# Optimization experiments

Hardware: AMD Instinct MI355X
Metric: run time of the kernel (lower is better)

## Reference

```python
import jax, jax.numpy as jnp
import numpy as np

N_NODES = 100000
N_EDGES = 3200000
F_IN = 128
F_OUT = 128


def setup_inputs() -> dict:
    key = jax.random.key(0)
    ks = jax.random.split(key, 6)
    stdv = 1.0 / np.sqrt(F_OUT)
    return {
        "x": jax.random.normal(ks[0], (N_NODES, F_IN), dtype=jnp.float32),
        "weight": jax.random.uniform(ks[1], (F_IN, F_OUT), minval=-stdv, maxval=stdv, dtype=jnp.float32),
        "bias": jax.random.uniform(ks[2], (F_OUT,), minval=-stdv, maxval=stdv, dtype=jnp.float32),
        "edge_src": jax.random.randint(ks[3], (N_EDGES,), 0, N_NODES, dtype=jnp.int32),
        "edge_dst": jax.random.randint(ks[4], (N_EDGES,), 0, N_NODES, dtype=jnp.int32),
        "edge_weight": jax.random.uniform(ks[5], (N_EDGES,), dtype=jnp.float32),
    }


def reference(x, weight, bias, edge_src, edge_dst, edge_weight):
    # Dense feature transform: support = X @ W  -> [N, F_OUT]
    support = jnp.matmul(x, weight)
    # Sparse adjacency aggregation (SpMM): out[d] = sum_e A[d, s_e] * support[s_e]
    msgs = support[edge_src] * edge_weight[:, None]  # [E, F_OUT]
    out = jax.ops.segment_sum(msgs, edge_dst, num_segments=N_NODES)
    return out + bias
```

## Files before the change

kernel.cpp:

```cpp
#include <hip/hip_runtime.h>

#define F 128
#define NB 64
#define MAXB 2048
#define NCHUNK 256

typedef __bf16 bf16x8 __attribute__((ext_vector_type(8)));
typedef unsigned short u16x8 __attribute__((ext_vector_type(8)));
typedef float f32x4 __attribute__((ext_vector_type(4)));

static __device__ __forceinline__ unsigned short f2bf(float f) {
    unsigned u = __float_as_uint(f);
    unsigned r = (u + 0x7FFF + ((u >> 16) & 1)) >> 16;
    return (unsigned short)r;
}

__global__ __launch_bounds__(256) void gemm_mfma_kernel(const float* __restrict__ X,
                                                        const float* __restrict__ W,
                                                        unsigned short* __restrict__ Sb,
                                                        int n_nodes) {
    __shared__ unsigned short WT[F * F];
    int t = threadIdx.x;
    {
        int f = t >> 1, half = t & 1;
#pragma unroll
        for (int j = 0; j < 8; ++j) {
            int k0 = half * 64 + j * 8;
            u16x8 pk;
#pragma unroll
            for (int i = 0; i < 8; ++i) pk[i] = f2bf(W[(size_t)(k0 + i) * F + f]);
            int byte = f * 256 + ((k0 * 2) ^ ((f & 7) << 4));
            *(u16x8*)((char*)WT + byte) = pk;
        }
    }
    __syncthreads();

    int w = t >> 6, l = t & 63;
    int lr = l & 15, lg = l >> 4;
    int rowBase = blockIdx.x * 64 + w * 16;

    f32x4 acc[8] = {};
    int a_row = rowBase + lr;
    if (a_row >= n_nodes) a_row = n_nodes - 1;
    const float* arow = X + (size_t)a_row * F + lg * 8;

#pragma unroll
    for (int kt = 0; kt < 4; ++kt) {
        const float* ap = arow + kt * 32;
        float4 x0 = *(const float4*)ap;
        float4 x1 = *(const float4*)(ap + 4);
        u16x8 au;
        au[0] = f2bf(x0.x); au[1] = f2bf(x0.y); au[2] = f2bf(x0.z); au[3] = f2bf(x0.w);
        au[4] = f2bf(x1.x); au[5] = f2bf(x1.y); au[6] = f2bf(x1.z); au[7] = f2bf(x1.w);
        bf16x8 a = __builtin_bit_cast(bf16x8, au);
#pragma unroll
        for (int ct = 0; ct < 8; ++ct) {
            int f = ct * 16 + lr;
            int byte = f * 256 + (((kt * 32 + lg * 8) * 2) ^ ((f & 7) << 4));
            bf16x8 b = *(bf16x8*)((char*)WT + byte);
            acc[ct] = __builtin_amdgcn_mfma_f32_16x16x32_bf16(a, b, acc[ct], 0, 0, 0);
        }
    }

#pragma unroll
    for (int ct = 0; ct < 8; ++ct) {
        int col = ct * 16 + lr;
#pragma unroll
        for (int j = 0; j < 4; ++j) {
            int row = rowBase + lg * 4 + j;
            if (row < n_nodes) Sb[(size_t)row * F + col] = f2bf(acc[ct][j]);
        }
    }
}

__global__ __launch_bounds__(256) void chunk_hist_kernel(const int* __restrict__ edst,
                                                         int* __restrict__ counts,
                                                         int* __restrict__ bcnt,
                                                         int n_edges, int nbuck, int epc) {
    __shared__ int h[MAXB];
    int c = blockIdx.x, t = threadIdx.x;
    for (int i = t; i < nbuck; i += 256) h[i] = 0;
    __syncthreads();
    int beg = c * epc, end = min(n_edges, beg + epc);
    for (int e = beg + t; e < end; e += 256) {
        atomicAdd(&h[edst[e] >> 6], 1);
    }
    __syncthreads();
    for (int i = t; i < nbuck; i += 256) {
        int v = h[i];
        counts[(size_t)c * nbuck + i] = v;
        if (v) __hip_atomic_fetch_add(&bcnt[i], v, __ATOMIC_RELAXED, __HIP_MEMORY_SCOPE_AGENT);
    }
}

__global__ __launch_bounds__(256) void bscan_kernel(const int* __restrict__ bcnt,
                                                    int* __restrict__ bstart, int nbuck) {
    __shared__ int tsum[256];
    int t = threadIdx.x;
    const int EPT = MAXB / 256;
    int base = t * EPT;
    int v[EPT];
    int s = 0;
#pragma unroll
    for (int i = 0; i < EPT; ++i) {
        int idx = base + i;
        v[i] = (idx < nbuck) ? bcnt[idx] : 0;
        s += v[i];
    }
    tsum[t] = s;
    __syncthreads();
    for (int off = 1; off < 256; off <<= 1) {
        int x = (t >= off) ? tsum[t - off] : 0;
        __syncthreads();
        tsum[t] += x;
        __syncthreads();
    }
    int run = tsum[t] - s;
#pragma unroll
    for (int i = 0; i < EPT; ++i) {
        int idx = base + i;
        if (idx < nbuck) {
            bstart[idx] = run;
            run += v[i];
        }
    }
    if (t == 255) bstart[nbuck] = run;
}

__global__ __launch_bounds__(64) void chunk_offs_kernel(const int* __restrict__ counts,
                                                        const int* __restrict__ bstart,
                                                        int* __restrict__ offs, int nbuck) {
    int b = blockIdx.x * 64 + threadIdx.x;
    if (b >= nbuck) return;
    int run = bstart[b];
    for (int c = 0; c < NCHUNK; ++c) {
        int v = counts[(size_t)c * nbuck + b];
        offs[(size_t)c * nbuck + b] = run;
        run += v;
    }
}

__global__ __launch_bounds__(256) void chunk_scatter_kernel(const int* __restrict__ esrc,
                                                            const int* __restrict__ edst,
                                                            const float* __restrict__ ew,
                                                            const int* __restrict__ offs,
                                                            int2* __restrict__ ebuf,
                                                            int n_edges, int nbuck, int epc) {
    __shared__ int lcur[MAXB];
    int c = blockIdx.x, t = threadIdx.x;
    for (int i = t; i < nbuck; i += 256) lcur[i] = offs[(size_t)c * nbuck + i];
    __syncthreads();
    int beg = c * epc, end = min(n_edges, beg + epc);
    for (int e = beg + t; e < end; e += 256) {
        int d = edst[e];
        int pos = atomicAdd(&lcur[d >> 6], 1);
        int2 p;
        p.x = esrc[e] | ((d & (NB - 1)) << 20);
        p.y = __float_as_int(ew[e]);
        ebuf[pos] = p;
    }
}

__global__ __launch_bounds__(256) void local_sort_kernel(const int2* __restrict__ ebuf,
                                                         const int* __restrict__ bstart,
                                                         int2* __restrict__ csr,
                                                         int* __restrict__ rowst,
                                                         int* __restrict__ cnt_out, int n_nodes) {
    __shared__ int lcnt[NB];
    __shared__ int lcur[NB];
    int b = blockIdx.x, t = threadIdx.x;
    int beg = bstart[b], end = bstart[b + 1];

    if (t < NB) lcnt[t] = 0;
    __syncthreads();

    for (int e = beg + t; e < end; e += 256) {
        int dl = (ebuf[e].x >> 20) & (NB - 1);
        atomicAdd(&lcnt[dl], 1);
    }
    __syncthreads();

    if (t < NB) {
        int v = lcnt[t];
        int inc = v;
#pragma unroll
        for (int off = 1; off < NB; off <<= 1) {
            int up = __shfl_up(inc, off, NB);
            if (t >= off) inc += up;
        }
        int excl = inc - v;
        lcur[t] = excl;
        int node = b * NB + t;
        if (node < n_nodes) {
            rowst[node] = beg + excl;
            cnt_out[node] = v;
        }
    }
    __syncthreads();

    for (int e = beg + t; e < end; e += 256) {
        int2 p = ebuf[e];
        int dl = (p.x >> 20) & (NB - 1);
        int pos = beg + atomicAdd(&lcur[dl], 1);
        int2 q;
        q.x = p.x & 0xFFFFF;
        q.y = p.y;
        csr[pos] = q;
    }
}

__global__ __launch_bounds__(256) void gather_kernel(const unsigned short* __restrict__ Sb,
                                                     const int2* __restrict__ csr,
                                                     const int* __restrict__ rowst,
                                                     const int* __restrict__ cnt,
                                                     const float* __restrict__ bias,
                                                     float* __restrict__ out, int n_nodes) {
    int node = blockIdx.x * 4 + (threadIdx.x >> 6);
    if (node >= n_nodes) return;
    int lane = threadIdx.x & 63;
    int f0 = lane * 2;

    float2 acc = *(const float2*)&bias[f0];
    int beg = rowst[node];
    int num = cnt[node];

    int i = 0;
    for (; i + 8 <= num; i += 8) {
        unsigned g[8];
        float wv[8];
#pragma unroll
        for (int j = 0; j < 8; ++j) {
            int2 p = csr[beg + i + j];
            g[j] = *(const unsigned*)(Sb + (size_t)p.x * F + f0);
            wv[j] = __int_as_float(p.y);
        }
#pragma unroll
        for (int j = 0; j < 8; ++j) {
            acc.x += wv[j] * __uint_as_float(g[j] << 16);
            acc.y += wv[j] * __uint_as_float(g[j] & 0xFFFF0000u);
        }
    }
    for (; i < num; ++i) {
        int2 p = csr[beg + i];
        unsigned g = *(const unsigned*)(Sb + (size_t)p.x * F + f0);
        float w = __int_as_float(p.y);
        acc.x += w * __uint_as_float(g << 16);
        acc.y += w * __uint_as_float(g & 0xFFFF0000u);
    }
    *(float2*)&out[(size_t)node * F + f0] = acc;
}

__global__ __launch_bounds__(256) void init_out_kernel(float* __restrict__ out,
                                                       const float* __restrict__ bias,
                                                       int n_nodes) {
    int idx = blockIdx.x * blockDim.x + threadIdx.x;
    int total = n_nodes * F;
    if (idx < total) out[idx] = bias[idx & (F - 1)];
}

__global__ __launch_bounds__(256) void scatter_edges_kernel(const unsigned short* __restrict__ Sb,
                                                            const int* __restrict__ esrc,
                                                            const int* __restrict__ edst,
                                                            const float* __restrict__ ew,
                                                            float* __restrict__ out,
                                                            int n_edges) {
    long long idx = (long long)blockIdx.x * blockDim.x + threadIdx.x;
    int e = (int)(idx >> 5);
    if (e >= n_edges) return;
    int fbase = ((int)idx & 31) * 4;
    int s = esrc[e];
    int d = edst[e];
    float w = ew[e];
    ushort4 v = *(const ushort4*)&Sb[(size_t)s * F + fbase];
    float* o = out + (size_t)d * F + fbase;
    __hip_atomic_fetch_add(&o[0], w * __uint_as_float((unsigned)v.x << 16), __ATOMIC_RELAXED, __HIP_MEMORY_SCOPE_AGENT);
    __hip_atomic_fetch_add(&o[1], w * __uint_as_float((unsigned)v.y << 16), __ATOMIC_RELAXED, __HIP_MEMORY_SCOPE_AGENT);
    __hip_atomic_fetch_add(&o[2], w * __uint_as_float((unsigned)v.z << 16), __ATOMIC_RELAXED, __HIP_MEMORY_SCOPE_AGENT);
    __hip_atomic_fetch_add(&o[3], w * __uint_as_float((unsigned)v.w << 16), __ATOMIC_RELAXED, __HIP_MEMORY_SCOPE_AGENT);
}

extern "C" void kernel_launch(void* const* d_in, const int* in_sizes, int n_in,
                              void* d_out, int out_size, void* d_ws, size_t ws_size,
                              hipStream_t stream) {
    const float* x    = (const float*)d_in[0];
    const float* w    = (const float*)d_in[1];
    const float* bias = (const float*)d_in[2];
    const int*   esrc = (const int*)d_in[3];
    const int*   edst = (const int*)d_in[4];
    const float* ew   = (const float*)d_in[5];
    float* out = (float*)d_out;

    int n_nodes = in_sizes[0] / F;
    int n_edges = in_sizes[3];
    int nbuck = (n_nodes + NB - 1) / NB;
    int epc = (n_edges + NCHUNK - 1) / NCHUNK;

    size_t off = 0;
    auto carve = [&](size_t bytes) -> void* {
        void* p = (char*)d_ws + off;
        off += (bytes + 255) & ~(size_t)255;
        return p;
    };
    unsigned short* Sb    = (unsigned short*)carve((size_t)n_nodes * F * sizeof(unsigned short));
    int2*           ebuf  = (int2*)carve((size_t)n_edges * sizeof(int2));
    int2*           csr   = (int2*)carve((size_t)n_edges * sizeof(int2));
    int*            bcnt  = (int*)carve((size_t)nbuck * sizeof(int));
    int*            bst   = (int*)carve((size_t)(nbuck + 1) * sizeof(int));
    int*            rowst = (int*)carve((size_t)n_nodes * sizeof(int));
    int*            ncnt  = (int*)carve((size_t)n_nodes * sizeof(int));
    int*            counts = (int*)carve((size_t)NCHUNK * nbuck * sizeof(int));
    int*            offs   = (int*)carve((size_t)NCHUNK * nbuck * sizeof(int));
    bool ok = (off <= ws_size) && (nbuck <= MAXB) && (n_nodes < (1 << 20));

    gemm_mfma_kernel<<<(n_nodes + 63) / 64, 256, 0, stream>>>(x, w, Sb, n_nodes);

    if (ok) {
        hipMemsetAsync(bcnt, 0, (size_t)nbuck * sizeof(int), stream);
        chunk_hist_kernel<<<NCHUNK, 256, 0, stream>>>(edst, counts, bcnt, n_edges, nbuck, epc);
        bscan_kernel<<<1, 256, 0, stream>>>(bcnt, bst, nbuck);
        chunk_offs_kernel<<<(nbuck + 63) / 64, 64, 0, stream>>>(counts, bst, offs, nbuck);
        chunk_scatter_kernel<<<NCHUNK, 256, 0, stream>>>(esrc, edst, ew, offs, ebuf,
                                                         n_edges, nbuck, epc);
        local_sort_kernel<<<nbuck, 256, 0, stream>>>(ebuf, bst, csr, rowst, ncnt, n_nodes);
        gather_kernel<<<(n_nodes + 3) / 4, 256, 0, stream>>>(Sb, csr, rowst, ncnt, bias, out,
                                                             n_nodes);
    } else {
        int total = n_nodes * F;
        init_out_kernel<<<(total + 255) / 256, 256, 0, stream>>>(out, bias, n_nodes);
        long long t2 = (long long)n_edges * 32;
        scatter_edges_kernel<<<(int)((t2 + 255) / 256), 256, 0, stream>>>(Sb, esrc, edst, ew, out,
                                                                          n_edges);
    }
}
```

Before: 252.1 us.

## Sort edges by source tile within rows, parallelize chunk offsets, nontemporal CSR loads

The local sort now keys each edge by destination node and by a coarse source-node tile (16 tiles). Within each row, gathered source rows are therefore ordered by source region, which should improve L2 locality across concurrent gather waves. The per-bucket chunk-offset scan now runs with 4 thread groups, each handling a quarter of the chunks with a shared-memory partial-sum combine, where before a single serial loop of 256 chunks ran per bucket. The gather reads CSR entries with nontemporal loads so they do not evict the support matrix from cache. The cost is a 1024-key block scan per bucket in local_sort.

```diff
diff --git a/kernel.cpp b/kernel.cpp
--- a/kernel.cpp
+++ b/kernel.cpp
@@ -4,6 +4,8 @@
 #define NB 64
 #define MAXB 2048
 #define NCHUNK 256
+#define NT 16
+#define KEYS (NB * NT)
 
 typedef __bf16 bf16x8 __attribute__((ext_vector_type(8)));
 typedef unsigned short u16x8 __attribute__((ext_vector_type(8)));
@@ -127,16 +129,27 @@
     if (t == 255) bstart[nbuck] = run;
 }
 
-__global__ __launch_bounds__(64) void chunk_offs_kernel(const int* __restrict__ counts,
-                                                        const int* __restrict__ bstart,
-                                                        int* __restrict__ offs, int nbuck) {
-    int b = blockIdx.x * 64 + threadIdx.x;
-    if (b >= nbuck) return;
-    int run = bstart[b];
-    for (int c = 0; c < NCHUNK; ++c) {
-        int v = counts[(size_t)c * nbuck + b];
-        offs[(size_t)c * nbuck + b] = run;
-        run += v;
+__global__ __launch_bounds__(256) void chunk_offs_kernel(const int* __restrict__ counts,
+                                                         const int* __restrict__ bstart,
+                                                         int* __restrict__ offs, int nbuck) {
+    __shared__ int part[4][64];
+    int t = threadIdx.x;
+    int q = t >> 6, bb = t & 63;
+    int b = blockIdx.x * 64 + bb;
+    int s = 0;
+    if (b < nbuck) {
+        for (int c = q * 64; c < q * 64 + 64; ++c) s += counts[(size_t)c * nbuck + b];
+    }
+    part[q][bb] = s;
+    __syncthreads();
+    if (b < nbuck) {
+        int run = bstart[b];
+        for (int qq = 0; qq < q; ++qq) run += part[qq][bb];
+        for (int c = q * 64; c < q * 64 + 64; ++c) {
+            size_t idx = (size_t)c * nbuck + b;
+            offs[idx] = run;
+            run += counts[idx];
+        }
     }
 }
 
@@ -165,45 +178,65 @@
                                                          const int* __restrict__ bstart,
                                                          int2* __restrict__ csr,
                                                          int* __restrict__ rowst,
-                                                         int* __restrict__ cnt_out, int n_nodes) {
-    __shared__ int lcnt[NB];
-    __shared__ int lcur[NB];
+                                                         int* __restrict__ cnt_out,
+                                                         int n_nodes, int ts) {
+    __shared__ int lcnt[KEYS];
+    __shared__ int lcur[KEYS];
+    __shared__ int tsum[256];
     int b = blockIdx.x, t = threadIdx.x;
     int beg = bstart[b], end = bstart[b + 1];
 
-    if (t < NB) lcnt[t] = 0;
+#pragma unroll
+    for (int i = t; i < KEYS; i += 256) lcnt[i] = 0;
     __syncthreads();
 
     for (int e = beg + t; e < end; e += 256) {
-        int dl = (ebuf[e].x >> 20) & (NB - 1);
-        atomicAdd(&lcnt[dl], 1);
+        int px = ebuf[e].x;
+        int key = ((px >> 20) & (NB - 1)) * NT + ((px & 0xFFFFF) >> ts);
+        atomicAdd(&lcnt[key], 1);
+    }
+    __syncthreads();
+
+    const int EPT = KEYS / 256;
+    int base = t * EPT;
+    int v[EPT];
+    int s = 0;
+#pragma unroll
+    for (int i = 0; i < EPT; ++i) { v[i] = lcnt[base + i]; s += v[i]; }
+    tsum[t] = s;
+    __syncthreads();
+    for (int off = 1; off < 256; off <<= 1) {
+        int x = (t >= off) ? tsum[t - off] : 0;
+        __syncthreads();
+        tsum[t] += x;
+        __syncthreads();
+    }
+    int run = tsum[t] - s;
+#pragma unroll
+    for (int i = 0; i < EPT; ++i) {
+        lcnt[base + i] = run;
+        lcur[base + i] = beg + run;
+        run += v[i];
     }
     __syncthreads();
 
     if (t < NB) {
-        int v = lcnt[t];
-        int inc = v;
-#pragma unroll
-        for (int off = 1; off < NB; off <<= 1) {
-            int up = __shfl_up(inc, off, NB);
-            if (t >= off) inc += up;
-        }
-        int excl = inc - v;
-        lcur[t] = excl;
         int node = b * NB + t;
         if (node < n_nodes) {
-            rowst[node] = beg + excl;
-            cnt_out[node] = v;
-        }
-    }
-    __syncthreads();
+            int p0 = lcnt[t * NT];
+            int p1 = (t == NB - 1) ? (end - beg) : lcnt[(t + 1) * NT];
+            rowst[node] = beg + p0;
+            cnt_out[node] = p1 - p0;
+        }
+    }
 
     for (int e = beg + t; e < end; e += 256) {
         int2 p = ebuf[e];
-        int dl = (p.x >> 20) & (NB - 1);
-        int pos = beg + atomicAdd(&lcur[dl], 1);
+        int src = p.x & 0xFFFFF;
+        int key = ((p.x >> 20) & (NB - 1)) * NT + (src >> ts);
+        int pos = atomicAdd(&lcur[key], 1);
         int2 q;
-        q.x = p.x & 0xFFFFF;
+        q.x = src;
         q.y = p.y;
         csr[pos] = q;
     }
@@ -230,9 +263,10 @@
         float wv[8];
 #pragma unroll
         for (int j = 0; j < 8; ++j) {
-            int2 p = csr[beg + i + j];
-            g[j] = *(const unsigned*)(Sb + (size_t)p.x * F + f0);
-            wv[j] = __int_as_float(p.y);
+            long long raw = __builtin_nontemporal_load((const long long*)&csr[beg + i + j]);
+            int srcj = (int)(raw & 0xFFFFFFFFll);
+            g[j] = *(const unsigned*)(Sb + (size_t)srcj * F + f0);
+            wv[j] = __int_as_float((int)(raw >> 32));
         }
 #pragma unroll
         for (int j = 0; j < 8; ++j) {
@@ -241,9 +275,10 @@
         }
     }
     for (; i < num; ++i) {
-        int2 p = csr[beg + i];
-        unsigned g = *(const unsigned*)(Sb + (size_t)p.x * F + f0);
-        float w = __int_as_float(p.y);
+        long long raw = __builtin_nontemporal_load((const long long*)&csr[beg + i]);
+        int srcj = (int)(raw & 0xFFFFFFFFll);
+        unsigned g = *(const unsigned*)(Sb + (size_t)srcj * F + f0);
+        float w = __int_as_float((int)(raw >> 32));
         acc.x += w * __uint_as_float(g << 16);
         acc.y += w * __uint_as_float(g & 0xFFFF0000u);
     }
@@ -295,6 +330,9 @@
     int nbuck = (n_nodes + NB - 1) / NB;
     int epc = (n_edges + NCHUNK - 1) / NCHUNK;
 
+    int ts = 0;
+    while (((n_nodes - 1) >> ts) >= NT) ++ts;
+
     size_t off = 0;
     auto carve = [&](size_t bytes) -> void* {
         void* p = (char*)d_ws + off;
@@ -318,10 +356,10 @@
         hipMemsetAsync(bcnt, 0, (size_t)nbuck * sizeof(int), stream);
         chunk_hist_kernel<<<NCHUNK, 256, 0, stream>>>(edst, counts, bcnt, n_edges, nbuck, epc);
         bscan_kernel<<<1, 256, 0, stream>>>(bcnt, bst, nbuck);
-        chunk_offs_kernel<<<(nbuck + 63) / 64, 64, 0, stream>>>(counts, bst, offs, nbuck);
+        chunk_offs_kernel<<<(nbuck + 63) / 64, 256, 0, stream>>>(counts, bst, offs, nbuck);
         chunk_scatter_kernel<<<NCHUNK, 256, 0, stream>>>(esrc, edst, ew, offs, ebuf,
                                                          n_edges, nbuck, epc);
-        local_sort_kernel<<<nbuck, 256, 0, stream>>>(ebuf, bst, csr, rowst, ncnt, n_nodes);
+        local_sort_kernel<<<nbuck, 256, 0, stream>>>(ebuf, bst, csr, rowst, ncnt, n_nodes, ts);
         gather_kernel<<<(n_nodes + 3) / 4, 256, 0, stream>>>(Sb, csr, rowst, ncnt, bias, out,
                                                              n_nodes);
     } else {
```

New measurement: 285.5 us. 1.13x slower.
